# Kernel tuning notes

Measured on AMD Instinct MI355X. Metric: run time of the kernel, lower is better.

Reference implementation:

```python
import jax, jax.numpy as jnp
import numpy as np

B, S, IN = 1024, 256, 8
H = 512
F = 96  # forecast_len
OUT = 1


def _lstm_step(h, c, x, Wih, Whh, bih, bhh):
    # PyTorch gate order: i, f, g, o
    gates = x @ Wih.T + h @ Whh.T + (bih + bhh)  # [B, 4H]
    i, f, g, o = jnp.split(gates, 4, axis=-1)
    i = jax.nn.sigmoid(i)
    f = jax.nn.sigmoid(f)
    g = jnp.tanh(g)
    o = jax.nn.sigmoid(o)
    c_new = f * c + i * g
    h_new = o * jnp.tanh(c_new)
    return h_new, c_new


def setup_inputs() -> dict:
    key = jax.random.key(0)
    ks = jax.random.split(key, 12)
    s_in = 1.0 / np.sqrt(H)
    def u(k, shape):
        return jax.random.uniform(k, shape, jnp.float32, -s_in, s_in)
    return {
        "x": jax.random.normal(ks[0], (B, S, IN), jnp.float32),
        "enc_Wih": u(ks[1], (4 * H, IN)),
        "enc_Whh": u(ks[2], (4 * H, H)),
        "enc_bih": u(ks[3], (4 * H,)),
        "enc_bhh": u(ks[4], (4 * H,)),
        "dec_Wih": u(ks[5], (4 * H, OUT)),
        "dec_Whh": u(ks[6], (4 * H, H)),
        "dec_bih": u(ks[7], (4 * H,)),
        "dec_bhh": u(ks[8], (4 * H,)),
        "out_W": u(ks[9], (OUT, H)),
        "out_b": u(ks[10], (OUT,)),
    }


def reference(x, enc_Wih, enc_Whh, enc_bih, enc_bhh,
              dec_Wih, dec_Whh, dec_bih, dec_bhh, out_W, out_b):
    batch = x.shape[0]
    h0 = jnp.zeros((batch, H), x.dtype)
    c0 = jnp.zeros((batch, H), x.dtype)

    # ---- Encoder: scan over time ----
    def enc_step(carry, xt):
        h, c = carry
        h, c = _lstm_step(h, c, xt, enc_Wih, enc_Whh, enc_bih, enc_bhh)
        return (h, c), None

    xs = jnp.swapaxes(x, 0, 1)  # [S, B, IN]
    (h, c), _ = jax.lax.scan(enc_step, (h0, c0), xs)

    y0 = jnp.zeros((batch, OUT), x.dtype)

    def dec_step(carry, _):
        h, c, y = carry
        h, c = _lstm_step(h, c, y, dec_Wih, dec_Whh, dec_bih, dec_bhh)
        pred = h @ out_W.T + out_b  # [B, 1]
        return (h, c, pred), pred

    _, preds = jax.lax.scan(dec_step, (h, c, y0), None, length=F)  # [F, B, 1]
    return jnp.swapaxes(preds[..., 0], 0, 1)  # [B, F]
```

## Files before the change

### kernel.cpp

```cpp
#include <hip/hip_runtime.h>


#define Hh 512
#define K2 544
#define BATCH 1024
#define SEQ 256
#define FCAST 96
#define SHS 40
#define HBP (16 * 64 * 64 * 8)

typedef _Float16 f16;
typedef _Float16 f16x8 __attribute__((ext_vector_type(8)));
typedef float f32x4 __attribute__((ext_vector_type(4)));

__device__ __forceinline__ float sigf(float v) { return 1.0f / (1.0f + __expf(-v)); }
__device__ __forceinline__ float tanhf_(float v) { return 1.0f - 2.0f / (__expf(2.0f * v) + 1.0f); }

__device__ __forceinline__ f16x8 ld16(const f16* p, bool byp) {
  f16x8 d;
  if (byp) asm volatile("global_load_dwordx4 %0, %1, off sc0 sc1" : "=&v"(d) : "v"(p) : "memory");
  else     asm volatile("global_load_dwordx4 %0, %1, off sc0"     : "=&v"(d) : "v"(p) : "memory");
  return d;
}
__device__ __forceinline__ void st16(f16* p, f16x8 v, bool byp) {
  if (byp) asm volatile("global_store_dwordx4 %0, %1, off sc0 sc1" :: "v"(p), "v"(v) : "memory");
  else     asm volatile("global_store_dwordx4 %0, %1, off"         :: "v"(p), "v"(v) : "memory");
}
__device__ __forceinline__ int atomic_add_l2(int* p, int v) {
  int old;
  asm volatile("global_atomic_add %0, %1, %2, off sc0\n\ts_waitcnt vmcnt(0)"
               : "=v"(old) : "v"(p), "v"(v) : "memory");
  return old;
}
__device__ __forceinline__ void wait_frags(f16x8 (&fr)[2][4]) {
  asm volatile("s_waitcnt vmcnt(0)"
               : "+v"(fr[0][0]), "+v"(fr[0][1]), "+v"(fr[0][2]), "+v"(fr[0][3]),
                 "+v"(fr[1][0]), "+v"(fr[1][1]), "+v"(fr[1][2]), "+v"(fr[1][3]));
}

__global__ void prep_weights(const float* __restrict__ encWih, const float* __restrict__ encWhh,
                             const float* __restrict__ decWih, const float* __restrict__ decWhh,
                             const float* __restrict__ encBih, const float* __restrict__ encBhh,
                             const float* __restrict__ decBih, const float* __restrict__ decBhh,
                             const float* __restrict__ outW, const float* __restrict__ outB,
                             f16* __restrict__ encT, f16* __restrict__ decPW, f16* __restrict__ decFW,
                             float* __restrict__ bE, float* __restrict__ bP, float* __restrict__ bF) {
  int id = blockIdx.x * 256 + threadIdx.x;
  if (id >= 2048 * 68) return;
  int n = id / 68, c8 = id % 68;
  int nslot = n >> 7, c = n & 127, w = c >> 5, cc = c & 31, ct = cc >> 4, l4v = cc & 15;
  int g = ct * 2 + (l4v >> 3), j = l4v & 7;
  int unit = nslot * 32 + w * 8 + j, r = g * Hh + unit;
  size_t o = (size_t)n * K2 + c8 * 8;
  if (c8 < 64) {
    float dwih = decWih[r];
#pragma unroll
    for (int e = 0; e < 8; ++e) {
      int k = c8 * 8 + e;
      encT[o + e] = (f16)encWhh[(size_t)r * Hh + k];
      float dw = decWhh[(size_t)r * Hh + k];
      decPW[o + e] = (f16)dw;
      decFW[o + e] = (f16)(dw + outW[k] * dwih);
    }
  } else if (c8 == 64) {
#pragma unroll
    for (int e = 0; e < 8; ++e) {
      encT[o + e] = (f16)encWih[r * 8 + e];
      decPW[o + e] = (f16)0.f;
      decFW[o + e] = (f16)0.f;
    }
  } else {
#pragma unroll
    for (int e = 0; e < 8; ++e) {
      encT[o + e] = (f16)0.f;
      decPW[o + e] = (f16)0.f;
      decFW[o + e] = (f16)0.f;
    }
  }
  if (c8 == 0) {
    bE[n] = encBih[r] + encBhh[r];
    float bd = decBih[r] + decBhh[r];
    bP[n] = bd;
    bF[n] = bd + outB[0] * decWih[r];
  }
}

__global__ void init_state(f16* __restrict__ hbuf, float* __restrict__ out,
                           const float* __restrict__ outB, int* __restrict__ sync) {
  int i = blockIdx.x * 256 + threadIdx.x;
  unsigned int* hb = (unsigned int*)hbuf;
  if (i < 524288) hb[i] = 0u;
  if (i < BATCH * FCAST) out[i] = outB[0];
  if (i < 2048) sync[i] = 0;
}

__global__ __launch_bounds__(256, 1) void lstm_persist(
    const f16* __restrict__ encT, const f16* __restrict__ decPW, const f16* __restrict__ decFW,
    const float* __restrict__ bE, const float* __restrict__ bP, const float* __restrict__ bF,
    const float* __restrict__ x, const float* __restrict__ outW,
    f16* __restrict__ hbuf, float* __restrict__ out, int* __restrict__ sync) {
  __shared__ __align__(16) f16 sH[64 * SHS];
  __shared__ int sInfo[2];

  int* cnt = sync;
  int* slots = sync + 1024;
  int* arrive = sync + 1032;

  const int T = threadIdx.x;
  const int w = T >> 6, lane = T & 63, l4 = lane & 15, q = lane >> 4;
  const int j = l4 & 7;
  const bool lo = (l4 < 8);

  int xcd;
  asm("s_getreg_b32 %0, hwreg(HW_REG_XCC_ID)" : "=s"(xcd));
  xcd &= 7;

  if (T == 0) {
    int r = __hip_atomic_fetch_add(&slots[xcd], 1, __ATOMIC_RELAXED, __HIP_MEMORY_SCOPE_AGENT);
    sInfo[0] = r;
    __hip_atomic_fetch_add(arrive, 1, __ATOMIC_RELAXED, __HIP_MEMORY_SCOPE_AGENT);
    while (__hip_atomic_load(arrive, __ATOMIC_RELAXED, __HIP_MEMORY_SCOPE_AGENT) < 256)
      __builtin_amdgcn_s_sleep(2);
    int ok = 1;
    for (int xx = 0; xx < 8; ++xx)
      ok &= (__hip_atomic_load(&slots[xx], __ATOMIC_RELAXED, __HIP_MEMORY_SCOPE_AGENT) == 32);
    sInfo[1] = ok;
  }
  __syncthreads();
  const int rank = sInfo[0];
  const bool uni = (sInfo[1] != 0);
  int group, nslot;
  if (uni) { group = xcd * 2 + (rank >> 4); nslot = rank & 15; }
  else     { group = (int)blockIdx.x >> 4;  nslot = (int)blockIdx.x & 15; }
  const int m0 = group * 64, n0 = nslot * 128, u0 = nslot * 32;
  int* myCnt = cnt + group * 32;

  f16x8 bw[2][17];
  float bias_r[4];
  float cst[2][4];
#pragma unroll
  for (int a = 0; a < 2; ++a)
#pragma unroll
    for (int r = 0; r < 4; ++r) cst[a][r] = 0.f;

  auto loadB = [&](const f16* WT, const float* bias) {
#pragma unroll
    for (int ct = 0; ct < 2; ++ct) {
      const f16* base = &WT[(size_t)(n0 + w * 32 + ct * 16 + l4) * K2 + q * 8];
#pragma unroll
      for (int ks = 0; ks < 17; ++ks) bw[ct][ks] = *(const f16x8*)(base + ks * 32);
    }
#pragma unroll
    for (int g = 0; g < 4; ++g)
      bias_r[g] = bias[n0 + w * 32 + (g >> 1) * 16 + (g & 1) * 8 + j];
  };

  loadB(encT, bE);
  float ow_r = 0.f;
  const int myUnit = u0 + w * 8 + j;
  const int fragBase = q * 512 + l4 * 8;

  for (int s = 0; s < SEQ + FCAST; ++s) {
    const bool enc = s < SEQ;
    if (s == SEQ) {
      loadB(decPW, bP);
      ow_r = outW[myUnit];
    } else if (s == SEQ + 1) {
      loadB(decFW, bF);
    }

    if (s > 0) {
      asm volatile("s_waitcnt vmcnt(0)" ::: "memory");
      __syncthreads();
      if (T == 0) {
        if (uni) {
          atomic_add_l2(myCnt, 1);
          while (atomic_add_l2(myCnt, 0) < 16 * s) __builtin_amdgcn_s_sleep(1);
        } else {
          __hip_atomic_fetch_add(myCnt, 1, __ATOMIC_RELAXED, __HIP_MEMORY_SCOPE_AGENT);
          while (__hip_atomic_load(myCnt, __ATOMIC_RELAXED, __HIP_MEMORY_SCOPE_AGENT) < 16 * s)
            __builtin_amdgcn_s_sleep(2);
        }
      }
      __syncthreads();
    }

    const int pin = s & 1, pout = pin ^ 1;
    const f16* hbL = hbuf + (size_t)pin * HBP + (size_t)group * 32768 + fragBase;
    f16* hbO = hbuf + (size_t)pout * HBP + (size_t)group * 32768;

    f32x4 acc[4][2];
#pragma unroll
    for (int a = 0; a < 4; ++a)
#pragma unroll
      for (int c = 0; c < 2; ++c) acc[a][c] = (f32x4){0.f, 0.f, 0.f, 0.f};

#pragma unroll
    for (int b = 0; b < 8; ++b) {
      f16x8 fr[2][4];
#pragma unroll
      for (int k2 = 0; k2 < 2; ++k2)
#pragma unroll
        for (int at = 0; at < 4; ++at)
          fr[k2][at] = ld16(&hbL[(b * 2 + k2) * 2048 + at * 128], !uni);
      wait_frags(fr);
#pragma unroll
      for (int k2 = 0; k2 < 2; ++k2) {
        const int ks = b * 2 + k2;
#pragma unroll
        for (int at = 0; at < 4; ++at) {
          acc[at][0] =
              __builtin_amdgcn_mfma_f32_16x16x32_f16(fr[k2][at], bw[0][ks], acc[at][0], 0, 0, 0);
          acc[at][1] =
              __builtin_amdgcn_mfma_f32_16x16x32_f16(fr[k2][at], bw[1][ks], acc[at][1], 0, 0, 0);
        }
      }
    }

    if (enc) {
#pragma unroll
      for (int at = 0; at < 4; ++at) {
        f16x8 af = {(f16)0.f, (f16)0.f, (f16)0.f, (f16)0.f,
                    (f16)0.f, (f16)0.f, (f16)0.f, (f16)0.f};
        if (q == 0) {
          const float* xp = &x[((size_t)(m0 + at * 16 + l4) * SEQ + s) * 8];
          float4 xa = *(const float4*)xp, xb = *(const float4*)(xp + 4);
          af = f16x8{(f16)xa.x, (f16)xa.y, (f16)xa.z, (f16)xa.w,
                     (f16)xb.x, (f16)xb.y, (f16)xb.z, (f16)xb.w};
        }
        acc[at][0] = __builtin_amdgcn_mfma_f32_16x16x32_f16(af, bw[0][16], acc[at][0], 0, 0, 0);
        acc[at][1] = __builtin_amdgcn_mfma_f32_16x16x32_f16(af, bw[1][16], acc[at][1], 0, 0, 0);
      }
    }

#pragma unroll
    for (int ah = 0; ah < 2; ++ah) {
#pragma unroll
      for (int r = 0; r < 4; ++r) {
        int atL = ah, atH = ah + 2;
        float xiL = acc[atL][0][r], xgL = acc[atL][1][r];
        float xiH = acc[atH][0][r], xgH = acc[atH][1][r];
        float payload0 = lo ? xiH : xiL;
        float payload1 = lo ? xgH : xgL;
        float recv0 = __shfl_xor(payload0, 8, 16);
        float recv1 = __shfl_xor(payload1, 8, 16);
        float pi = (lo ? xiL : recv0) + bias_r[0];
        float pf = (lo ? recv0 : xiH) + bias_r[1];
        float pg = (lo ? xgL : recv1) + bias_r[2];
        float po = (lo ? recv1 : xgH) + bias_r[3];
        float ig = sigf(pi), fg = sigf(pf), gg = tanhf_(pg), og = sigf(po);
        float cn = fg * cst[ah][r] + ig * gg;
        cst[ah][r] = cn;
        float hn = og * tanhf_(cn);
        int at = lo ? atL : atH;
        int row = at * 16 + q * 4 + r;
        sH[row * SHS + w * 8 + j] = (f16)hn;
        if (!enc) {
          float pp = hn * ow_r;
          pp += __shfl_xor(pp, 1, 16);
          pp += __shfl_xor(pp, 2, 16);
          pp += __shfl_xor(pp, 4, 16);
          if (j == 0) atomicAdd(&out[(m0 + row) * FCAST + (s - SEQ)], pp);
        }
      }
    }
    __syncthreads();

    {
      int row = lane, seg = w;
      f16x8 hv = *(const f16x8*)&sH[row * SHS + seg * 8];
      st16(&hbO[((nslot * 4 + seg) * 64 + row) * 8], hv, !uni);
    }
  }
}

extern "C" void kernel_launch(void* const* d_in, const int* in_sizes, int n_in, void* d_out,
                              int out_size, void* d_ws, size_t ws_size, hipStream_t stream) {
  const float* x = (const float*)d_in[0];
  const float* encWih = (const float*)d_in[1];
  const float* encWhh = (const float*)d_in[2];
  const float* encBih = (const float*)d_in[3];
  const float* encBhh = (const float*)d_in[4];
  const float* decWih = (const float*)d_in[5];
  const float* decWhh = (const float*)d_in[6];
  const float* decBih = (const float*)d_in[7];
  const float* decBhh = (const float*)d_in[8];
  const float* outW = (const float*)d_in[9];
  const float* outB = (const float*)d_in[10];
  float* out = (float*)d_out;

  char* ws = (char*)d_ws;
  f16* encT = (f16*)ws;
  f16* decPW = encT + 2048 * K2;
  f16* decFW = decPW + 2048 * K2;
  f16* hbuf = decFW + 2048 * K2;
  float* bE = (float*)(hbuf + 2 * HBP);
  float* bP = bE + 2048;
  float* bF = bP + 2048;
  int* sync = (int*)(bF + 2048);

  prep_weights<<<544, 256, 0, stream>>>(encWih, encWhh, decWih, decWhh, encBih, encBhh, decBih,
                                        decBhh, outW, outB, encT, decPW, decFW, bE, bP, bF);
  init_state<<<2048, 256, 0, stream>>>(hbuf, out, outB, sync);
  lstm_persist<<<256, 256, 0, stream>>>(encT, decPW, decFW, bE, bP, bF, x, outW, hbuf, out, sync);
}
```

Measured before the change: 2.718 ms.

## Split batch rows into two halves with separate barriers to overlap step sync

```diff
diff --git a/kernel.cpp b/kernel.cpp
--- a/kernel.cpp
+++ b/kernel.cpp
@@ -7,7 +7,7 @@
 #define SEQ 256
 #define FCAST 96
 #define SHS 40
-#define HBP (16 * 64 * 64 * 8)
+#define HBP (16 * 32768)
 
 typedef _Float16 f16;
 typedef _Float16 f16x8 __attribute__((ext_vector_type(8)));
@@ -32,10 +32,10 @@
                : "=v"(old) : "v"(p), "v"(v) : "memory");
   return old;
 }
-__device__ __forceinline__ void wait_frags(f16x8 (&fr)[2][4]) {
+__device__ __forceinline__ void wait_frags8(f16x8 (&fr)[4][2]) {
   asm volatile("s_waitcnt vmcnt(0)"
-               : "+v"(fr[0][0]), "+v"(fr[0][1]), "+v"(fr[0][2]), "+v"(fr[0][3]),
-                 "+v"(fr[1][0]), "+v"(fr[1][1]), "+v"(fr[1][2]), "+v"(fr[1][3]));
+               : "+v"(fr[0][0]), "+v"(fr[0][1]), "+v"(fr[1][0]), "+v"(fr[1][1]),
+                 "+v"(fr[2][0]), "+v"(fr[2][1]), "+v"(fr[3][0]), "+v"(fr[3][1]));
 }
 
 __global__ void prep_weights(const float* __restrict__ encWih, const float* __restrict__ encWhh,
@@ -133,7 +133,7 @@
   if (uni) { group = xcd * 2 + (rank >> 4); nslot = rank & 15; }
   else     { group = (int)blockIdx.x >> 4;  nslot = (int)blockIdx.x & 15; }
   const int m0 = group * 64, n0 = nslot * 128, u0 = nslot * 32;
-  int* myCnt = cnt + group * 32;
+  int* myCnt = cnt + group * 64;
 
   f16x8 bw[2][17];
   float bias_r[4];
@@ -158,7 +158,7 @@
   loadB(encT, bE);
   float ow_r = 0.f;
   const int myUnit = u0 + w * 8 + j;
-  const int fragBase = q * 512 + l4 * 8;
+  const int fragBase = q * 256 + l4 * 8;
 
   for (int s = 0; s < SEQ + FCAST; ++s) {
     const bool enc = s < SEQ;
@@ -169,77 +169,74 @@
       loadB(decFW, bF);
     }
 
-    if (s > 0) {
-      asm volatile("s_waitcnt vmcnt(0)" ::: "memory");
-      __syncthreads();
-      if (T == 0) {
-        if (uni) {
-          atomic_add_l2(myCnt, 1);
-          while (atomic_add_l2(myCnt, 0) < 16 * s) __builtin_amdgcn_s_sleep(1);
-        } else {
-          __hip_atomic_fetch_add(myCnt, 1, __ATOMIC_RELAXED, __HIP_MEMORY_SCOPE_AGENT);
-          while (__hip_atomic_load(myCnt, __ATOMIC_RELAXED, __HIP_MEMORY_SCOPE_AGENT) < 16 * s)
-            __builtin_amdgcn_s_sleep(2);
+    const int pin = s & 1, pout = pin ^ 1;
+    const f16* hbG = hbuf + (size_t)pin * HBP + (size_t)group * 32768;
+    f16* hbO = hbuf + (size_t)pout * HBP + (size_t)group * 32768;
+
+#pragma unroll
+    for (int hf = 0; hf < 2; ++hf) {
+      int* cH = myCnt + hf * 32;
+
+      if (s > 0) {
+        if (T == 0) {
+          if (uni) {
+            while (atomic_add_l2(cH, 0) < 16 * s) __builtin_amdgcn_s_sleep(1);
+          } else {
+            while (__hip_atomic_load(cH, __ATOMIC_RELAXED, __HIP_MEMORY_SCOPE_AGENT) < 16 * s)
+              __builtin_amdgcn_s_sleep(2);
+          }
         }
-      }
-      __syncthreads();
-    }
-
-    const int pin = s & 1, pout = pin ^ 1;
-    const f16* hbL = hbuf + (size_t)pin * HBP + (size_t)group * 32768 + fragBase;
-    f16* hbO = hbuf + (size_t)pout * HBP + (size_t)group * 32768;
-
-    f32x4 acc[4][2];
-#pragma unroll
-    for (int a = 0; a < 4; ++a)
-#pragma unroll
-      for (int c = 0; c < 2; ++c) acc[a][c] = (f32x4){0.f, 0.f, 0.f, 0.f};
-
-#pragma unroll
-    for (int b = 0; b < 8; ++b) {
-      f16x8 fr[2][4];
-#pragma unroll
-      for (int k2 = 0; k2 < 2; ++k2)
-#pragma unroll
-        for (int at = 0; at < 4; ++at)
-          fr[k2][at] = ld16(&hbL[(b * 2 + k2) * 2048 + at * 128], !uni);
-      wait_frags(fr);
-#pragma unroll
-      for (int k2 = 0; k2 < 2; ++k2) {
-        const int ks = b * 2 + k2;
-#pragma unroll
-        for (int at = 0; at < 4; ++at) {
-          acc[at][0] =
-              __builtin_amdgcn_mfma_f32_16x16x32_f16(fr[k2][at], bw[0][ks], acc[at][0], 0, 0, 0);
-          acc[at][1] =
-              __builtin_amdgcn_mfma_f32_16x16x32_f16(fr[k2][at], bw[1][ks], acc[at][1], 0, 0, 0);
+        __syncthreads();
+      }
+
+      const f16* hp = hbG + hf * 16384 + fragBase;
+      f32x4 acc[2][2];
+#pragma unroll
+      for (int a = 0; a < 2; ++a)
+#pragma unroll
+        for (int c = 0; c < 2; ++c) acc[a][c] = (f32x4){0.f, 0.f, 0.f, 0.f};
+
+#pragma unroll
+      for (int b = 0; b < 4; ++b) {
+        f16x8 fr[4][2];
+#pragma unroll
+        for (int k4 = 0; k4 < 4; ++k4)
+#pragma unroll
+          for (int atl = 0; atl < 2; ++atl)
+            fr[k4][atl] = ld16(&hp[(b * 4 + k4) * 1024 + atl * 128], !uni);
+        wait_frags8(fr);
+#pragma unroll
+        for (int k4 = 0; k4 < 4; ++k4) {
+          const int ks = b * 4 + k4;
+#pragma unroll
+          for (int atl = 0; atl < 2; ++atl) {
+            acc[atl][0] =
+                __builtin_amdgcn_mfma_f32_16x16x32_f16(fr[k4][atl], bw[0][ks], acc[atl][0], 0, 0, 0);
+            acc[atl][1] =
+                __builtin_amdgcn_mfma_f32_16x16x32_f16(fr[k4][atl], bw[1][ks], acc[atl][1], 0, 0, 0);
+          }
         }
       }
-    }
-
-    if (enc) {
-#pragma unroll
-      for (int at = 0; at < 4; ++at) {
-        f16x8 af = {(f16)0.f, (f16)0.f, (f16)0.f, (f16)0.f,
-                    (f16)0.f, (f16)0.f, (f16)0.f, (f16)0.f};
-        if (q == 0) {
-          const float* xp = &x[((size_t)(m0 + at * 16 + l4) * SEQ + s) * 8];
-          float4 xa = *(const float4*)xp, xb = *(const float4*)(xp + 4);
-          af = f16x8{(f16)xa.x, (f16)xa.y, (f16)xa.z, (f16)xa.w,
-                     (f16)xb.x, (f16)xb.y, (f16)xb.z, (f16)xb.w};
+      if (enc) {
+#pragma unroll
+        for (int atl = 0; atl < 2; ++atl) {
+          f16x8 af = {(f16)0.f, (f16)0.f, (f16)0.f, (f16)0.f,
+                      (f16)0.f, (f16)0.f, (f16)0.f, (f16)0.f};
+          if (q == 0) {
+            const float* xp = &x[((size_t)(m0 + (2 * hf + atl) * 16 + l4) * SEQ + s) * 8];
+            float4 xa = *(const float4*)xp, xb = *(const float4*)(xp + 4);
+            af = f16x8{(f16)xa.x, (f16)xa.y, (f16)xa.z, (f16)xa.w,
+                       (f16)xb.x, (f16)xb.y, (f16)xb.z, (f16)xb.w};
+          }
+          acc[atl][0] = __builtin_amdgcn_mfma_f32_16x16x32_f16(af, bw[0][16], acc[atl][0], 0, 0, 0);
+          acc[atl][1] = __builtin_amdgcn_mfma_f32_16x16x32_f16(af, bw[1][16], acc[atl][1], 0, 0, 0);
         }
-        acc[at][0] = __builtin_amdgcn_mfma_f32_16x16x32_f16(af, bw[0][16], acc[at][0], 0, 0, 0);
-        acc[at][1] = __builtin_amdgcn_mfma_f32_16x16x32_f16(af, bw[1][16], acc[at][1], 0, 0, 0);
-      }
-    }
-
-#pragma unroll
-    for (int ah = 0; ah < 2; ++ah) {
+      }
+
 #pragma unroll
       for (int r = 0; r < 4; ++r) {
-        int atL = ah, atH = ah + 2;
-        float xiL = acc[atL][0][r], xgL = acc[atL][1][r];
-        float xiH = acc[atH][0][r], xgH = acc[atH][1][r];
+        float xiL = acc[0][0][r], xgL = acc[0][1][r];
+        float xiH = acc[1][0][r], xgH = acc[1][1][r];
         float payload0 = lo ? xiH : xiL;
         float payload1 = lo ? xgH : xgL;
         float recv0 = __shfl_xor(payload0, 8, 16);
@@ -249,10 +246,10 @@
         float pg = (lo ? xgL : recv1) + bias_r[2];
         float po = (lo ? recv1 : xgH) + bias_r[3];
         float ig = sigf(pi), fg = sigf(pf), gg = tanhf_(pg), og = sigf(po);
-        float cn = fg * cst[ah][r] + ig * gg;
-        cst[ah][r] = cn;
+        float cn = fg * cst[hf][r] + ig * gg;
+        cst[hf][r] = cn;
         float hn = og * tanhf_(cn);
-        int at = lo ? atL : atH;
+        int at = lo ? (2 * hf) : (2 * hf + 1);
         int row = at * 16 + q * 4 + r;
         sH[row * SHS + w * 8 + j] = (f16)hn;
         if (!enc) {
@@ -263,13 +260,19 @@
           if (j == 0) atomicAdd(&out[(m0 + row) * FCAST + (s - SEQ)], pp);
         }
       }
-    }
-    __syncthreads();
-
-    {
-      int row = lane, seg = w;
-      f16x8 hv = *(const f16x8*)&sH[row * SHS + seg * 8];
-      st16(&hbO[((nslot * 4 + seg) * 64 + row) * 8], hv, !uni);
+      __syncthreads();
+
+      if (T < 128) {
+        int row32 = T & 31, seg = T >> 5;
+        f16x8 hv = *(const f16x8*)&sH[(32 * hf + row32) * SHS + seg * 8];
+        st16(&hbO[hf * 16384 + nslot * 1024 + seg * 256 + row32 * 8], hv, !uni);
+      }
+      asm volatile("s_waitcnt vmcnt(0)" ::: "memory");
+      __syncthreads();
+      if (T == 0) {
+        if (uni) atomic_add_l2(cH, 1);
+        else __hip_atomic_fetch_add(cH, 1, __ATOMIC_RELAXED, __HIP_MEMORY_SCOPE_AGENT);
+      }
     }
   }
 }
```

Result: slower. 2.970 ms (+9.3%).

## Split per-step group barrier into per-quarter readiness counters overlapping with MMA

Applied to the files above, without the earlier changes.

```diff
diff --git a/kernel.cpp b/kernel.cpp
--- a/kernel.cpp
+++ b/kernel.cpp
@@ -7,7 +7,7 @@
 #define SEQ 256
 #define FCAST 96
 #define SHS 40
-#define HBP (16 * 64 * 64 * 8)
+#define HBP (16 * 32768)
 
 typedef _Float16 f16;
 typedef _Float16 f16x8 __attribute__((ext_vector_type(8)));
@@ -32,7 +32,7 @@
                : "=v"(old) : "v"(p), "v"(v) : "memory");
   return old;
 }
-__device__ __forceinline__ void wait_frags(f16x8 (&fr)[2][4]) {
+__device__ __forceinline__ void wait_frags8(f16x8 (&fr)[2][4]) {
   asm volatile("s_waitcnt vmcnt(0)"
                : "+v"(fr[0][0]), "+v"(fr[0][1]), "+v"(fr[0][2]), "+v"(fr[0][3]),
                  "+v"(fr[1][0]), "+v"(fr[1][1]), "+v"(fr[1][2]), "+v"(fr[1][3]));
@@ -91,7 +91,7 @@
   unsigned int* hb = (unsigned int*)hbuf;
   if (i < 524288) hb[i] = 0u;
   if (i < BATCH * FCAST) out[i] = outB[0];
-  if (i < 2048) sync[i] = 0;
+  if (i < 8192) sync[i] = 0;
 }
 
 __global__ __launch_bounds__(256, 1) void lstm_persist(
@@ -101,10 +101,10 @@
     f16* __restrict__ hbuf, float* __restrict__ out, int* __restrict__ sync) {
   __shared__ __align__(16) f16 sH[64 * SHS];
   __shared__ int sInfo[2];
-
-  int* cnt = sync;
-  int* slots = sync + 1024;
-  int* arrive = sync + 1032;
+  __shared__ int sFlag[4];
+
+  int* slots = sync + 4096;
+  int* arrive = sync + 4104;
 
   const int T = threadIdx.x;
   const int w = T >> 6, lane = T & 63, l4 = lane & 15, q = lane >> 4;
@@ -126,6 +126,7 @@
       ok &= (__hip_atomic_load(&slots[xx], __ATOMIC_RELAXED, __HIP_MEMORY_SCOPE_AGENT) == 32);
     sInfo[1] = ok;
   }
+  if (T < 4) sFlag[T] = 0;
   __syncthreads();
   const int rank = sInfo[0];
   const bool uni = (sInfo[1] != 0);
@@ -133,7 +134,8 @@
   if (uni) { group = xcd * 2 + (rank >> 4); nslot = rank & 15; }
   else     { group = (int)blockIdx.x >> 4;  nslot = (int)blockIdx.x & 15; }
   const int m0 = group * 64, n0 = nslot * 128, u0 = nslot * 32;
-  int* myCnt = cnt + group * 32;
+  int* qC = sync + group * 256;
+  int* tC = qC + 128;
 
   f16x8 bw[2][17];
   float bias_r[4];
@@ -169,22 +171,6 @@
       loadB(decFW, bF);
     }
 
-    if (s > 0) {
-      asm volatile("s_waitcnt vmcnt(0)" ::: "memory");
-      __syncthreads();
-      if (T == 0) {
-        if (uni) {
-          atomic_add_l2(myCnt, 1);
-          while (atomic_add_l2(myCnt, 0) < 16 * s) __builtin_amdgcn_s_sleep(1);
-        } else {
-          __hip_atomic_fetch_add(myCnt, 1, __ATOMIC_RELAXED, __HIP_MEMORY_SCOPE_AGENT);
-          while (__hip_atomic_load(myCnt, __ATOMIC_RELAXED, __HIP_MEMORY_SCOPE_AGENT) < 16 * s)
-            __builtin_amdgcn_s_sleep(2);
-        }
-      }
-      __syncthreads();
-    }
-
     const int pin = s & 1, pout = pin ^ 1;
     const f16* hbL = hbuf + (size_t)pin * HBP + (size_t)group * 32768 + fragBase;
     f16* hbO = hbuf + (size_t)pout * HBP + (size_t)group * 32768;
@@ -197,13 +183,32 @@
 
 #pragma unroll
     for (int b = 0; b < 8; ++b) {
+      if (s > 0 && (b & 1) == 0) {
+        const int qd = b >> 1;
+        if (w == 0) {
+          if (lane == 0) {
+            if (uni) {
+              while (atomic_add_l2(qC + qd * 32, 0) < 4 * s) __builtin_amdgcn_s_sleep(1);
+            } else {
+              while (__hip_atomic_load(qC + qd * 32, __ATOMIC_RELAXED,
+                                       __HIP_MEMORY_SCOPE_AGENT) < 4 * s)
+                __builtin_amdgcn_s_sleep(2);
+            }
+            __hip_atomic_store(&sFlag[qd], s, __ATOMIC_RELAXED, __HIP_MEMORY_SCOPE_WORKGROUP);
+          }
+        } else {
+          while (__hip_atomic_load(&sFlag[qd], __ATOMIC_RELAXED,
+                                   __HIP_MEMORY_SCOPE_WORKGROUP) < s)
+            ;
+        }
+      }
       f16x8 fr[2][4];
 #pragma unroll
       for (int k2 = 0; k2 < 2; ++k2)
 #pragma unroll
         for (int at = 0; at < 4; ++at)
           fr[k2][at] = ld16(&hbL[(b * 2 + k2) * 2048 + at * 128], !uni);
-      wait_frags(fr);
+      wait_frags8(fr);
 #pragma unroll
       for (int k2 = 0; k2 < 2; ++k2) {
         const int ks = b * 2 + k2;
@@ -264,12 +269,33 @@
         }
       }
     }
+
+    if (s > 0 && T == 0) {
+      if (uni) {
+        while (atomic_add_l2(tC, 0) < 16 * s) __builtin_amdgcn_s_sleep(1);
+      } else {
+        while (__hip_atomic_load(tC, __ATOMIC_RELAXED, __HIP_MEMORY_SCOPE_AGENT) < 16 * s)
+          __builtin_amdgcn_s_sleep(2);
+      }
+    }
     __syncthreads();
 
     {
       int row = lane, seg = w;
       f16x8 hv = *(const f16x8*)&sH[row * SHS + seg * 8];
       st16(&hbO[((nslot * 4 + seg) * 64 + row) * 8], hv, !uni);
+    }
+    asm volatile("s_waitcnt vmcnt(0)" ::: "memory");
+    __syncthreads();
+    if (T == 0) {
+      if (uni) {
+        atomic_add_l2(qC + (nslot >> 2) * 32, 1);
+        atomic_add_l2(tC, 1);
+      } else {
+        __hip_atomic_fetch_add(qC + (nslot >> 2) * 32, 1, __ATOMIC_RELAXED,
+                               __HIP_MEMORY_SCOPE_AGENT);
+        __hip_atomic_fetch_add(tC, 1, __ATOMIC_RELAXED, __HIP_MEMORY_SCOPE_AGENT);
+      }
     }
   }
 }
```

After: 3.087 ms. 13.6% more time.

## Halve batch rows per block and run two persistent blocks per CU

Applied to the files above, without the earlier changes.

```diff
diff --git a/kernel.cpp b/kernel.cpp
--- a/kernel.cpp
+++ b/kernel.cpp
@@ -7,7 +7,7 @@
 #define SEQ 256
 #define FCAST 96
 #define SHS 40
-#define HBP (16 * 64 * 64 * 8)
+#define HBP (32 * 16384)
 
 typedef _Float16 f16;
 typedef _Float16 f16x8 __attribute__((ext_vector_type(8)));
@@ -32,10 +32,9 @@
                : "=v"(old) : "v"(p), "v"(v) : "memory");
   return old;
 }
-__device__ __forceinline__ void wait_frags(f16x8 (&fr)[2][4]) {
+__device__ __forceinline__ void wait_frags4(f16x8 (&fr)[2][2]) {
   asm volatile("s_waitcnt vmcnt(0)"
-               : "+v"(fr[0][0]), "+v"(fr[0][1]), "+v"(fr[0][2]), "+v"(fr[0][3]),
-                 "+v"(fr[1][0]), "+v"(fr[1][1]), "+v"(fr[1][2]), "+v"(fr[1][3]));
+               : "+v"(fr[0][0]), "+v"(fr[0][1]), "+v"(fr[1][0]), "+v"(fr[1][1]));
 }
 
 __global__ void prep_weights(const float* __restrict__ encWih, const float* __restrict__ encWhh,
@@ -91,20 +90,20 @@
   unsigned int* hb = (unsigned int*)hbuf;
   if (i < 524288) hb[i] = 0u;
   if (i < BATCH * FCAST) out[i] = outB[0];
-  if (i < 2048) sync[i] = 0;
-}
-
-__global__ __launch_bounds__(256, 1) void lstm_persist(
+  if (i < 8192) sync[i] = 0;
+}
+
+__global__ __launch_bounds__(256, 2) void lstm_persist(
     const f16* __restrict__ encT, const f16* __restrict__ decPW, const f16* __restrict__ decFW,
     const float* __restrict__ bE, const float* __restrict__ bP, const float* __restrict__ bF,
     const float* __restrict__ x, const float* __restrict__ outW,
     f16* __restrict__ hbuf, float* __restrict__ out, int* __restrict__ sync) {
-  __shared__ __align__(16) f16 sH[64 * SHS];
+  __shared__ __align__(16) f16 sH[32 * SHS];
   __shared__ int sInfo[2];
 
   int* cnt = sync;
-  int* slots = sync + 1024;
-  int* arrive = sync + 1032;
+  int* slots = sync + 4096;
+  int* arrive = sync + 4104;
 
   const int T = threadIdx.x;
   const int w = T >> 6, lane = T & 63, l4 = lane & 15, q = lane >> 4;
@@ -119,29 +118,27 @@
     int r = __hip_atomic_fetch_add(&slots[xcd], 1, __ATOMIC_RELAXED, __HIP_MEMORY_SCOPE_AGENT);
     sInfo[0] = r;
     __hip_atomic_fetch_add(arrive, 1, __ATOMIC_RELAXED, __HIP_MEMORY_SCOPE_AGENT);
-    while (__hip_atomic_load(arrive, __ATOMIC_RELAXED, __HIP_MEMORY_SCOPE_AGENT) < 256)
+    while (__hip_atomic_load(arrive, __ATOMIC_RELAXED, __HIP_MEMORY_SCOPE_AGENT) < 512)
       __builtin_amdgcn_s_sleep(2);
     int ok = 1;
     for (int xx = 0; xx < 8; ++xx)
-      ok &= (__hip_atomic_load(&slots[xx], __ATOMIC_RELAXED, __HIP_MEMORY_SCOPE_AGENT) == 32);
+      ok &= (__hip_atomic_load(&slots[xx], __ATOMIC_RELAXED, __HIP_MEMORY_SCOPE_AGENT) == 64);
     sInfo[1] = ok;
   }
   __syncthreads();
   const int rank = sInfo[0];
   const bool uni = (sInfo[1] != 0);
   int group, nslot;
-  if (uni) { group = xcd * 2 + (rank >> 4); nslot = rank & 15; }
+  if (uni) { group = xcd * 4 + (rank >> 4); nslot = rank & 15; }
   else     { group = (int)blockIdx.x >> 4;  nslot = (int)blockIdx.x & 15; }
-  const int m0 = group * 64, n0 = nslot * 128, u0 = nslot * 32;
-  int* myCnt = cnt + group * 32;
+  const int m0 = group * 32, n0 = nslot * 128, u0 = nslot * 32;
+  int* myCnt = cnt + group * 64;
 
   f16x8 bw[2][17];
   float bias_r[4];
-  float cst[2][4];
-#pragma unroll
-  for (int a = 0; a < 2; ++a)
-#pragma unroll
-    for (int r = 0; r < 4; ++r) cst[a][r] = 0.f;
+  float cst[4];
+#pragma unroll
+  for (int r = 0; r < 4; ++r) cst[r] = 0.f;
 
   auto loadB = [&](const f16* WT, const float* bias) {
 #pragma unroll
@@ -158,7 +155,7 @@
   loadB(encT, bE);
   float ow_r = 0.f;
   const int myUnit = u0 + w * 8 + j;
-  const int fragBase = q * 512 + l4 * 8;
+  const int fragBase = q * 256 + l4 * 8;
 
   for (int s = 0; s < SEQ + FCAST; ++s) {
     const bool enc = s < SEQ;
@@ -170,14 +167,10 @@
     }
 
     if (s > 0) {
-      asm volatile("s_waitcnt vmcnt(0)" ::: "memory");
-      __syncthreads();
       if (T == 0) {
         if (uni) {
-          atomic_add_l2(myCnt, 1);
           while (atomic_add_l2(myCnt, 0) < 16 * s) __builtin_amdgcn_s_sleep(1);
         } else {
-          __hip_atomic_fetch_add(myCnt, 1, __ATOMIC_RELAXED, __HIP_MEMORY_SCOPE_AGENT);
           while (__hip_atomic_load(myCnt, __ATOMIC_RELAXED, __HIP_MEMORY_SCOPE_AGENT) < 16 * s)
             __builtin_amdgcn_s_sleep(2);
         }
@@ -186,29 +179,29 @@
     }
 
     const int pin = s & 1, pout = pin ^ 1;
-    const f16* hbL = hbuf + (size_t)pin * HBP + (size_t)group * 32768 + fragBase;
-    f16* hbO = hbuf + (size_t)pout * HBP + (size_t)group * 32768;
-
-    f32x4 acc[4][2];
-#pragma unroll
-    for (int a = 0; a < 4; ++a)
+    const f16* hbL = hbuf + (size_t)pin * HBP + (size_t)group * 16384 + fragBase;
+    f16* hbO = hbuf + (size_t)pout * HBP + (size_t)group * 16384;
+
+    f32x4 acc[2][2];
+#pragma unroll
+    for (int a = 0; a < 2; ++a)
 #pragma unroll
       for (int c = 0; c < 2; ++c) acc[a][c] = (f32x4){0.f, 0.f, 0.f, 0.f};
 
 #pragma unroll
     for (int b = 0; b < 8; ++b) {
-      f16x8 fr[2][4];
+      f16x8 fr[2][2];
 #pragma unroll
       for (int k2 = 0; k2 < 2; ++k2)
 #pragma unroll
-        for (int at = 0; at < 4; ++at)
-          fr[k2][at] = ld16(&hbL[(b * 2 + k2) * 2048 + at * 128], !uni);
-      wait_frags(fr);
+        for (int at = 0; at < 2; ++at)
+          fr[k2][at] = ld16(&hbL[(b * 2 + k2) * 1024 + at * 128], !uni);
+      wait_frags4(fr);
 #pragma unroll
       for (int k2 = 0; k2 < 2; ++k2) {
         const int ks = b * 2 + k2;
 #pragma unroll
-        for (int at = 0; at < 4; ++at) {
+        for (int at = 0; at < 2; ++at) {
           acc[at][0] =
               __builtin_amdgcn_mfma_f32_16x16x32_f16(fr[k2][at], bw[0][ks], acc[at][0], 0, 0, 0);
           acc[at][1] =
@@ -219,7 +212,7 @@
 
     if (enc) {
 #pragma unroll
-      for (int at = 0; at < 4; ++at) {
+      for (int at = 0; at < 2; ++at) {
         f16x8 af = {(f16)0.f, (f16)0.f, (f16)0.f, (f16)0.f,
                     (f16)0.f, (f16)0.f, (f16)0.f, (f16)0.f};
         if (q == 0) {
@@ -234,42 +227,44 @@
     }
 
 #pragma unroll
-    for (int ah = 0; ah < 2; ++ah) {
-#pragma unroll
-      for (int r = 0; r < 4; ++r) {
-        int atL = ah, atH = ah + 2;
-        float xiL = acc[atL][0][r], xgL = acc[atL][1][r];
-        float xiH = acc[atH][0][r], xgH = acc[atH][1][r];
-        float payload0 = lo ? xiH : xiL;
-        float payload1 = lo ? xgH : xgL;
-        float recv0 = __shfl_xor(payload0, 8, 16);
-        float recv1 = __shfl_xor(payload1, 8, 16);
-        float pi = (lo ? xiL : recv0) + bias_r[0];
-        float pf = (lo ? recv0 : xiH) + bias_r[1];
-        float pg = (lo ? xgL : recv1) + bias_r[2];
-        float po = (lo ? recv1 : xgH) + bias_r[3];
-        float ig = sigf(pi), fg = sigf(pf), gg = tanhf_(pg), og = sigf(po);
-        float cn = fg * cst[ah][r] + ig * gg;
-        cst[ah][r] = cn;
-        float hn = og * tanhf_(cn);
-        int at = lo ? atL : atH;
-        int row = at * 16 + q * 4 + r;
-        sH[row * SHS + w * 8 + j] = (f16)hn;
-        if (!enc) {
-          float pp = hn * ow_r;
-          pp += __shfl_xor(pp, 1, 16);
-          pp += __shfl_xor(pp, 2, 16);
-          pp += __shfl_xor(pp, 4, 16);
-          if (j == 0) atomicAdd(&out[(m0 + row) * FCAST + (s - SEQ)], pp);
-        }
+    for (int r = 0; r < 4; ++r) {
+      float xiL = acc[0][0][r], xgL = acc[0][1][r];
+      float xiH = acc[1][0][r], xgH = acc[1][1][r];
+      float payload0 = lo ? xiH : xiL;
+      float payload1 = lo ? xgH : xgL;
+      float recv0 = __shfl_xor(payload0, 8, 16);
+      float recv1 = __shfl_xor(payload1, 8, 16);
+      float pi = (lo ? xiL : recv0) + bias_r[0];
+      float pf = (lo ? recv0 : xiH) + bias_r[1];
+      float pg = (lo ? xgL : recv1) + bias_r[2];
+      float po = (lo ? recv1 : xgH) + bias_r[3];
+      float ig = sigf(pi), fg = sigf(pf), gg = tanhf_(pg), og = sigf(po);
+      float cn = fg * cst[r] + ig * gg;
+      cst[r] = cn;
+      float hn = og * tanhf_(cn);
+      int at = lo ? 0 : 1;
+      int row = at * 16 + q * 4 + r;
+      sH[row * SHS + w * 8 + j] = (f16)hn;
+      if (!enc) {
+        float pp = hn * ow_r;
+        pp += __shfl_xor(pp, 1, 16);
+        pp += __shfl_xor(pp, 2, 16);
+        pp += __shfl_xor(pp, 4, 16);
+        if (j == 0) atomicAdd(&out[(m0 + row) * FCAST + (s - SEQ)], pp);
       }
     }
     __syncthreads();
 
-    {
-      int row = lane, seg = w;
-      f16x8 hv = *(const f16x8*)&sH[row * SHS + seg * 8];
-      st16(&hbO[((nslot * 4 + seg) * 64 + row) * 8], hv, !uni);
+    if (T < 128) {
+      int row32 = T & 31, seg = T >> 5;
+      f16x8 hv = *(const f16x8*)&sH[row32 * SHS + seg * 8];
+      st16(&hbO[nslot * 1024 + seg * 256 + row32 * 8], hv, !uni);
+    }
+    asm volatile("s_waitcnt vmcnt(0)" ::: "memory");
+    __syncthreads();
+    if (T == 0) {
+      if (uni) atomic_add_l2(myCnt, 1);
+      else __hip_atomic_fetch_add(myCnt, 1, __ATOMIC_RELAXED, __HIP_MEMORY_SCOPE_AGENT);
     }
   }
 }
@@ -302,5 +297,5 @@
   prep_weights<<<544, 256, 0, stream>>>(encWih, encWhh, decWih, decWhh, encBih, encBhh, decBih,
                                         decBhh, outW, outB, encT, decPW, decFW, bE, bP, bF);
   init_state<<<2048, 256, 0, stream>>>(hbuf, out, outB, sync);
-  lstm_persist<<<256, 256, 0, stream>>>(encT, decPW, decFW, bE, bP, bF, x, outW, hbuf, out, sync);
-}
+  lstm_persist<<<512, 256, 0, stream>>>(encT, decPW, decFW, bE, bP, bF, x, outW, hbuf, out, sync);
+}
```

New measurement: 3.780 ms. +39.1%, slower.
